# Optimization experiments

Measured on AMD Instinct MI355X. Metric: run time of the kernel, lower is better.

## Reference

```python
import jax, jax.numpy as jnp
import numpy as np

# dims: F=N_fault, V=N_train (noise samples), E=batch, M=n_in+2, N=n_out
F, V, E, N_IN, N_OUT = 2, 4, 2048, 512, 512
M = N_IN + 2
GMIN, GMAX, EPS_TRAIN, PGMIN = 0.01, 10.0, 0.1, 1e-4
ETA2_ACT1 = 0.20  # ACT1.eta_fault[0,2], used in theta init
# pTanh activation params per ACT: a = e0 + e1*tanh((z-e2)*e3)
ETAS = np.array([[0.05, 0.90, 0.20, 8.0],
                 [0.10, 0.80, 0.30, 5.0],
                 [0.00, 1.00, 0.25, 10.0],
                 [0.15, 0.70, 0.15, 6.0]], dtype=np.float32)


def setup_inputs() -> dict:
    key = jax.random.key(0)
    k1, k2, k3, k4, k5 = jax.random.split(key, 5)
    a_previous = jax.random.uniform(k1, (F, V, E, N_IN), jnp.float32)
    # theta init per __init__: rand/100 + gmin; last row += gmax; row -2 from eta_2 formula
    theta = jax.random.uniform(k2, (M, N_OUT), jnp.float32) / 100.0 + GMIN
    theta = theta.at[-1, :].add(GMAX)
    theta = theta.at[-2, :].set(ETA2_ACT1 / (1.0 - ETA2_ACT1) * (jnp.sum(theta[:-2, :], 0) + theta[-1, :]))
    cofficients_act = jax.random.uniform(k3, (4, N_OUT), jnp.float32)
    noise_u = jax.random.uniform(k4, (F, V, M, N_OUT), jnp.float32)   # theta_noisy uniform draw
    gumbel_u = jax.random.uniform(k5, (4, N_OUT), jnp.float32)        # gumbel uniform draw
    return {"a_previous": a_previous, "theta_": theta,
            "cofficients_act": cofficients_act, "noise_u": noise_u, "gumbel_u": gumbel_u}


def _forward(a_previous, theta_, cofficients_act, noise_u, gumbel_u):
    sg = jax.lax.stop_gradient
    # --- theta property: clamp to [-gmax,gmax], zero |.|<gmin, straight-through ---
    th_c = jnp.clip(theta_, -GMAX, GMAX)
    th_t = jnp.where(jnp.abs(th_c) < GMIN, 0.0, th_c)
    theta = sg(th_t) + theta_ - sg(theta_)
    # --- theta_noisy: multiplicative uniform noise in [1-eps, 1+eps]; FaultMask == 1 ---
    theta_noisy = theta[None, None] * ((noise_u * 2.0 - 1.0) * EPS_TRAIN + 1.0)  # [F,V,M,N]
    absn = jnp.abs(theta_noisy)
    W = absn / (jnp.sum(absn, axis=2, keepdims=True) + 1e-10)
    pos = (theta_noisy >= 0).astype(theta_noisy.dtype)
    neg = 1.0 - pos
    # --- MAC: extend input with [ones, zeros], inverter path, split-sign matmul ---
    ones = jnp.ones(a_previous.shape[:3] + (1,), a_previous.dtype)
    zeros = jnp.zeros_like(ones)
    x_ext = jnp.concatenate([a_previous, ones, zeros], axis=3)  # [F,V,E,M]
    x_neg = (-x_ext).at[..., -1].set(0.0)                       # ideal INV(a) = -a, last col zeroed
    z = (jnp.einsum('fvem,fvmn->fven', x_ext, W * pos)
         + jnp.einsum('fvem,fvmn->fven', x_neg, W * neg))       # [F,V,E,N]
    # --- MAC_power: vectorized form of the quad loop ---
    # Power = sum_{f,v,m,n} g[m,n] * sum_e (x_ext*pos + x_neg*neg - y)^2 / (E*V*F)
    # pos*neg = 0, pos^2 = pos  =>  expand the square into einsum reductions.
    g_init = jnp.abs(th_c)
    g_tilde = g_init * (PGMIN / jnp.min(g_init, axis=0, keepdims=True))
    pos_d, neg_d = sg(pos), sg(neg)  # detached in torch source
    sx2 = jnp.einsum('fvem,fvem->fvm', x_ext, x_ext)
    sn2 = jnp.einsum('fvem,fvem->fvm', x_neg, x_neg)
    sy2 = jnp.einsum('fven,fven->fvn', z, z)
    C = jnp.einsum('fvem,fven->fvmn', x_ext, z)
    D = jnp.einsum('fvem,fven->fvmn', x_neg, z)
    p1 = (jnp.einsum('fvm,fvmn,mn->', sx2, pos_d, g_tilde)
          + jnp.einsum('fvm,fvmn,mn->', sn2, neg_d, g_tilde))
    p2 = -2.0 * (jnp.einsum('fvmn,fvmn,mn->', C, pos_d, g_tilde)
                 + jnp.einsum('fvmn,fvmn,mn->', D, neg_d, g_tilde))
    p3 = jnp.einsum('fvn,n->', sy2, jnp.sum(g_tilde, axis=0))
    mac_power = (p1 + p2 + p3) / (E * V * F)
    # --- CoFF_ACT: clamped logits + gumbel, softmax, hard argmax straight-through ---
    c = cofficients_act + sg(jnp.clip(cofficients_act, -1.0, 1.0) - cofficients_act)
    gn = -jnp.log(-jnp.log(gumbel_u + 1e-20) + 1e-20)
    alpha = jax.nn.softmax((c + gn) / 1.0, axis=0)              # temperature = 1.0
    hard = jax.nn.one_hot(jnp.argmax(alpha, axis=0), 4, axis=0, dtype=alpha.dtype)
    alpha_st = sg(hard) + alpha - sg(alpha)                      # [4, N]
    # --- mix the four pTanh activations ---
    a_new = jnp.zeros_like(z)
    for i in range(4):
        e0, e1, e2, e3 = ETAS[i]
        a_new = a_new + alpha_st[i] * (e0 + e1 * jnp.tanh((z - e2) * e3))
    return a_new, mac_power


def reference(a_previous, theta_, cofficients_act, noise_u, gumbel_u):
    return _forward(a_previous, theta_, cofficients_act, noise_u, gumbel_u)
```

## Files before the change

### kernel.cpp

```cpp
#include <hip/hip_runtime.h>

typedef unsigned short u16;
typedef __attribute__((ext_vector_type(8))) short short8;
typedef __attribute__((ext_vector_type(4))) float f32x4;

#define NF 2
#define NV 4
#define FV 8
#define NE 2048
#define NIN 512
#define NOUT 512
#define NM 514

#define WS_P1      0u
#define WS_P2      2048u
#define WS_P3      3072u
#define WS_SCALE   4096u
#define WS_G       6144u
#define WS_GN      8320u
#define WS_ETA     10368u
#define WS_BIASZ   18560u
#define WS_BIAST   34944u
#define WS_DENP    51328u
#define WS_PMIN    133248u
#define WS_PSUM    264320u
#define WS_ABF     395392u
#define WS_BZT     17172608u
#define WS_BTT     21366912u

__constant__ float c_etas[4][4] = {
    {0.05f, 0.90f, 0.20f, 8.0f},
    {0.10f, 0.80f, 0.30f, 5.0f},
    {0.00f, 1.00f, 0.25f, 10.0f},
    {0.15f, 0.70f, 0.15f, 6.0f}};

__device__ __forceinline__ u16 f2bf(float x) {
    unsigned u = __float_as_uint(x);
    unsigned r = (u + 0x7fffu + ((u >> 16) & 1u)) >> 16;
    return (u16)r;
}

__device__ __forceinline__ void gll16(const void* g, void* l) {
    __builtin_amdgcn_global_load_lds((__attribute__((address_space(1))) void*)g,
                                     (__attribute__((address_space(3))) void*)l,
                                     16, 0, 0);
}

__global__ void kA_part(const float* __restrict__ theta_, float* __restrict__ pmin,
                        float* __restrict__ psum) {
    int t = threadIdx.x;
    int n2 = t * 2;
    int r0 = blockIdx.x * 9;
    float mn0 = 3.4e38f, mn1 = 3.4e38f, s0 = 0.f, s1 = 0.f;
    int rend = r0 + 9;
    if (rend > NM) rend = NM;
    for (int r = r0; r < rend; r++) {
        float2 v = *(const float2*)(theta_ + r * NOUT + n2);
        float a0 = fabsf(fminf(fmaxf(v.x, -10.f), 10.f));
        float a1 = fabsf(fminf(fmaxf(v.y, -10.f), 10.f));
        mn0 = fminf(mn0, a0); mn1 = fminf(mn1, a1);
        s0 += a0; s1 += a1;
    }
    *(float2*)(pmin + blockIdx.x * NOUT + n2) = make_float2(mn0, mn1);
    *(float2*)(psum + blockIdx.x * NOUT + n2) = make_float2(s0, s1);
}

__global__ void kB_fold(const float* __restrict__ pmin, const float* __restrict__ psum,
                        const float* __restrict__ coeff, const float* __restrict__ gumb,
                        float* __restrict__ scale, float* __restrict__ Gn,
                        float4* __restrict__ eta4) {
    int n = threadIdx.x;
    float mn = 3.4e38f, s = 0.f;
    for (int i = 0; i < 64; i++) {
        mn = fminf(mn, pmin[i * NOUT + n]);
        s += psum[i * NOUT + n];
    }
    float sc = 1e-4f / mn;
    scale[n] = sc;
    Gn[n] = sc * s;
    float best = -1e30f;
    int bi = 0;
    for (int i = 0; i < 4; i++) {
        float c = fminf(fmaxf(coeff[i * NOUT + n], -1.f), 1.f);
        float u = gumb[i * NOUT + n];
        float g = -logf(-logf(u + 1e-20f) + 1e-20f);
        float v = c + g;
        if (v > best) { best = v; bi = i; }
    }
    eta4[n] = make_float4(c_etas[bi][0], c_etas[bi][1], c_etas[bi][2], c_etas[bi][3]);
}

__global__ void kC_grow(const float* __restrict__ theta_, const float* __restrict__ scale,
                        float* __restrict__ G) {
    int m = blockIdx.x;
    int t = threadIdx.x;
    const float4* rowp = (const float4*)(theta_ + m * NOUT);
    const float4* scp = (const float4*)scale;
    float acc = 0.f;
#pragma unroll
    for (int i = 0; i < 2; i++) {
        float4 v = rowp[t * 2 + i];
        float4 s = scp[t * 2 + i];
        acc += fabsf(fminf(fmaxf(v.x, -10.f), 10.f)) * s.x
             + fabsf(fminf(fmaxf(v.y, -10.f), 10.f)) * s.y
             + fabsf(fminf(fmaxf(v.z, -10.f), 10.f)) * s.z
             + fabsf(fminf(fmaxf(v.w, -10.f), 10.f)) * s.w;
    }
    for (int off = 32; off > 0; off >>= 1) acc += __shfl_down(acc, off);
    if (t == 0) G[m] = acc;
}

__global__ void k_denomp(const float* __restrict__ theta_, const float* __restrict__ noise,
                         float* __restrict__ denomp) {
    int fv = blockIdx.z, mc = blockIdx.y, nc = blockIdx.x;
    int t = threadIdx.x;
    int nl = t & 63, mg = t >> 6;
    int n = nc * 64 + nl;
    int mbase = mc * 128 + mg * 32;
    float acc = 0.f;
    for (int i = 0; i < 32; i++) {
        int m = mbase + i;
        if (m < NM) {
            float fac = noise[(fv * NM + m) * NOUT + n] * 0.2f + 0.9f;
            float thc = fminf(fmaxf(theta_[m * NOUT + n], -10.f), 10.f);
            float tht = (fabsf(thc) < 0.01f) ? 0.f : thc;
            acc += fabsf(tht * fac);
        }
    }
    __shared__ float red[4][64];
    red[mg][nl] = acc;
    __syncthreads();
    if (t < 64)
        denomp[(mc * FV + fv) * NOUT + nc * 64 + t] =
            red[0][t] + red[1][t] + red[2][t] + red[3][t];
}

__global__ void k_wmat3(const float* __restrict__ theta_, const float* __restrict__ scale,
                        const float* __restrict__ noise, const float* __restrict__ denomp,
                        u16* __restrict__ BzT, u16* __restrict__ BtT,
                        float* __restrict__ bias_z, float* __restrict__ bias_t) {
    int fv = blockIdx.z, mt = blockIdx.y, nt = blockIdx.x;
    int t = threadIdx.x;
    int nl = t & 63, rg = t >> 6;
    __shared__ u16 Wl[64][66];
    __shared__ u16 Sl[64][66];
    int n = nt * 64 + nl;
    float dsum = 1e-10f;
#pragma unroll
    for (int mc = 0; mc < 5; mc++) dsum += denomp[(mc * FV + fv) * NOUT + n];
    float rdv = 1.f / dsum;
    float sc = scale[n];
    for (int r = 0; r < 16; r++) {
        int ml = rg * 16 + r;
        int m = mt * 64 + ml;
        if (m < 513) {
            float fac = noise[(fv * NM + m) * NOUT + n] * 0.2f + 0.9f;
            float thc = fminf(fmaxf(theta_[m * NOUT + n], -10.f), 10.f);
            float gi = fabsf(thc);
            float tht = (gi < 0.01f) ? 0.f : thc;
            float th = tht * fac;
            float sg = (th >= 0.f) ? 1.f : -1.f;
            float gt = gi * sc;
            if (m == 512) {
                bias_z[fv * NOUT + n] = th * rdv;
                bias_t[fv * NOUT + n] = sg * gt;
            } else {
                Wl[ml][nl] = f2bf(th * rdv);
                Sl[ml][nl] = f2bf(sg * gt);
            }
        }
    }
    __syncthreads();
    if (mt < 8) {
        for (int r = 0; r < 16; r++) {
            int nl2 = rg * 16 + r;
            int ml2 = t & 63;
            int gidx = (fv * NOUT + nt * 64 + nl2) * NIN + mt * 64 + ml2;
            BzT[gidx] = Wl[ml2][nl2];
            BtT[gidx] = Sl[ml2][nl2];
        }
    }
}

__global__ void k_prepA(const float* __restrict__ a_prev, const float* __restrict__ G,
                        u16* __restrict__ Abf, float* __restrict__ p1slot) {
    int t = threadIdx.x;
    float acc = 0.f;
#pragma unroll
    for (int i = 0; i < 4; i++) {
        int idx = (i * 2048 + blockIdx.x) * 256 + t;
        float4 v = ((const float4*)a_prev)[idx];
        int k = (idx & 127) << 2;
        float4 g4 = *((const float4*)(G + k));
        acc += v.x * v.x * g4.x + v.y * v.y * g4.y + v.z * v.z * g4.z + v.w * v.w * g4.w;
        ushort4 o;
        o.x = f2bf(v.x); o.y = f2bf(v.y); o.z = f2bf(v.z); o.w = f2bf(v.w);
        ((ushort4*)Abf)[idx] = o;
    }
    for (int off = 32; off > 0; off >>= 1) acc += __shfl_down(acc, off);
    __shared__ float red[4];
    int lane = t & 63, wv = t >> 6;
    if (lane == 0) red[wv] = acc;
    __syncthreads();
    if (t == 0)
        atomicAdd(&p1slot[(blockIdx.x & 63) * 8], red[0] + red[1] + red[2] + red[3]);
}

__global__ __launch_bounds__(256, 2) void k_gemm(
    const u16* __restrict__ Abf, const u16* __restrict__ BzT, const u16* __restrict__ BtT,
    const float* __restrict__ bias_z, const float* __restrict__ bias_t,
    const float* __restrict__ Gn, const float4* __restrict__ eta4,
    float* __restrict__ out, float* __restrict__ p2slot, float* __restrict__ p3slot) {
    __shared__ alignas(16) u16 As[128 * 64];
    __shared__ alignas(16) u16 Bzs[128 * 64];
    __shared__ alignas(16) u16 Bts[128 * 64];
    const int tid = threadIdx.x;
    const int lane = tid & 63;
    const int wv = tid >> 6;
    const int wr = wv >> 1, wc = wv & 1;
    const int fv = blockIdx.z;
    const int e0 = blockIdx.y * 128;
    const int n0 = blockIdx.x * 128;

    const u16* Ag = Abf + (fv * NE + e0) * NIN;
    const u16* Bzg = BzT + (fv * NOUT + n0) * NIN;
    const u16* Btg = BtT + (fv * NOUT + n0) * NIN;

    f32x4 accz[4][4], acct[4][4];
#pragma unroll
    for (int i = 0; i < 4; i++)
#pragma unroll
        for (int j = 0; j < 4; j++) {
            f32x4 zz = {0.f, 0.f, 0.f, 0.f};
            accz[i][j] = zz;
            acct[i][j] = zz;
        }

    const int srow = tid >> 3;
    const int swz = (((tid & 7) ^ (srow & 7))) * 8;

    for (int k0 = 0; k0 < 512; k0 += 64) {
#pragma unroll
        for (int i = 0; i < 4; i++) {
            int so = (i * 32 + srow) * 512 + k0 + swz;
            int dof = i * 2048 + tid * 8;
            gll16(Ag + so, (u16*)As + dof);
            gll16(Bzg + so, (u16*)Bzs + dof);
            gll16(Btg + so, (u16*)Bts + dof);
        }
        __builtin_amdgcn_s_waitcnt(0);
        __syncthreads();
        const int rA = wr * 64 + (lane & 15);
        const int rB = wc * 64 + (lane & 15);
#pragma unroll
        for (int s = 0; s < 2; s++) {
            const int ca = ((s * 4 + (lane >> 4)) ^ (lane & 7)) * 8;
            short8 af[4], bzf[4], btf[4];
#pragma unroll
            for (int i = 0; i < 4; i++) af[i] = *(const short8*)(As + (rA + i * 16) * 64 + ca);
#pragma unroll
            for (int j = 0; j < 4; j++) {
                bzf[j] = *(const short8*)(Bzs + (rB + j * 16) * 64 + ca);
                btf[j] = *(const short8*)(Bts + (rB + j * 16) * 64 + ca);
            }
#pragma unroll
            for (int i = 0; i < 4; i++)
#pragma unroll
                for (int j = 0; j < 4; j++) {
                    accz[i][j] = __builtin_amdgcn_mfma_f32_16x16x32_bf16(af[i], bzf[j], accz[i][j], 0, 0, 0);
                    acct[i][j] = __builtin_amdgcn_mfma_f32_16x16x32_bf16(af[i], btf[j], acct[i][j], 0, 0, 0);
                }
        }
        __syncthreads();
    }

    float p2 = 0.f, p3 = 0.f;
    const int col = lane & 15;
    const int rowq = (lane >> 4) * 4;
#pragma unroll
    for (int j = 0; j < 4; j++) {
        int n = n0 + wc * 64 + j * 16 + col;
        float bz = bias_z[fv * NOUT + n];
        float bt = bias_t[fv * NOUT + n];
        float gnv = Gn[n];
        float4 e4 = eta4[n];
#pragma unroll
        for (int i = 0; i < 4; i++) {
            int ebase = e0 + wr * 64 + i * 16 + rowq;
#pragma unroll
            for (int r = 0; r < 4; r++) {
                float z = accz[i][j][r] + bz;
                float t = acct[i][j][r] + bt;
                p2 += z * t;
                p3 += z * z * gnv;
                float x = (z - e4.z) * e4.w;
                float ex = __expf(2.f * x);
                float th = 1.f - 2.f / (ex + 1.f);
                out[(fv * NE + ebase + r) * NOUT + n] = e4.x + e4.y * th;
            }
        }
    }
    for (int off = 32; off > 0; off >>= 1) {
        p2 += __shfl_down(p2, off);
        p3 += __shfl_down(p3, off);
    }
    __shared__ float r2[4], r3[4];
    if (lane == 0) { r2[wv] = p2; r3[wv] = p3; }
    __syncthreads();
    if (tid == 0) {
        int slot = ((blockIdx.x + blockIdx.y * 4 + blockIdx.z * 64) & 31) * 8;
        atomicAdd(&p2slot[slot], r2[0] + r2[1] + r2[2] + r2[3]);
        atomicAdd(&p3slot[slot], r3[0] + r3[1] + r3[2] + r3[3]);
    }
}

__global__ void k_final(const float* __restrict__ p1s, const float* __restrict__ p2s,
                        const float* __restrict__ p3s, const float* __restrict__ G,
                        float* __restrict__ out) {
    int t = threadIdx.x;
    float s1 = p1s[t * 8];
    float s2 = (t < 32) ? p2s[t * 8] : 0.f;
    float s3 = (t < 32) ? p3s[t * 8] : 0.f;
    for (int off = 32; off > 0; off >>= 1) {
        s1 += __shfl_down(s1, off);
        s2 += __shfl_down(s2, off);
        s3 += __shfl_down(s3, off);
    }
    if (t == 0) {
        float mp = (s1 + 16384.f * G[512] - 2.f * s2 + s3) * (1.f / 16384.f);
        out[8388608] = mp;
    }
}

extern "C" void kernel_launch(void* const* d_in, const int* in_sizes, int n_in,
                              void* d_out, int out_size, void* d_ws, size_t ws_size,
                              hipStream_t stream) {
    const float* a_prev = (const float*)d_in[0];
    const float* theta_ = (const float*)d_in[1];
    const float* coeff = (const float*)d_in[2];
    const float* noise = (const float*)d_in[3];
    const float* gumb = (const float*)d_in[4];
    float* out = (float*)d_out;
    char* w = (char*)d_ws;
    float* p1s = (float*)(w + WS_P1);
    float* p2s = (float*)(w + WS_P2);
    float* p3s = (float*)(w + WS_P3);
    float* scale = (float*)(w + WS_SCALE);
    float* G = (float*)(w + WS_G);
    float* Gn = (float*)(w + WS_GN);
    float4* eta4 = (float4*)(w + WS_ETA);
    float* bias_z = (float*)(w + WS_BIASZ);
    float* bias_t = (float*)(w + WS_BIAST);
    float* denomp = (float*)(w + WS_DENP);
    float* pmin = (float*)(w + WS_PMIN);
    float* psum = (float*)(w + WS_PSUM);
    u16* Abf = (u16*)(w + WS_ABF);
    u16* BzT = (u16*)(w + WS_BZT);
    u16* BtT = (u16*)(w + WS_BTT);

    hipMemsetAsync(w + WS_P1, 0, 4096, stream);

    kA_part<<<64, 256, 0, stream>>>(theta_, pmin, psum);
    kB_fold<<<1, 512, 0, stream>>>(pmin, psum, coeff, gumb, scale, Gn, eta4);
    kC_grow<<<514, 64, 0, stream>>>(theta_, scale, G);
    k_denomp<<<dim3(8, 5, FV), 256, 0, stream>>>(theta_, noise, denomp);
    k_wmat3<<<dim3(8, 9, FV), 256, 0, stream>>>(theta_, scale, noise, denomp,
                                                BzT, BtT, bias_z, bias_t);
    k_prepA<<<2048, 256, 0, stream>>>(a_prev, G, Abf, p1s);
    k_gemm<<<dim3(4, 16, FV), 256, 0, stream>>>(Abf, BzT, BtT, bias_z, bias_t, Gn, eta4,
                                                out, p2s, p3s);
    k_final<<<1, 64, 0, stream>>>(p1s, p2s, p3s, G, out);
}
```

Baseline: 153.1 us.

## Defer column normalization to GEMM epilogue and vectorize weight prep kernels

```diff
diff --git a/kernel.cpp b/kernel.cpp
--- a/kernel.cpp
+++ b/kernel.cpp
@@ -22,11 +22,11 @@
 #define WS_BIASZ   18560u
 #define WS_BIAST   34944u
 #define WS_DENP    51328u
-#define WS_PMIN    133248u
-#define WS_PSUM    264320u
-#define WS_ABF     395392u
-#define WS_BZT     17172608u
-#define WS_BTT     21366912u
+#define WS_PMIN    182400u
+#define WS_PSUM    313472u
+#define WS_ABF     444544u
+#define WS_BZT     17221760u
+#define WS_BTT     21416064u
 
 __constant__ float c_etas[4][4] = {
     {0.05f, 0.90f, 0.20f, 8.0f},
@@ -112,73 +112,88 @@
 
 __global__ void k_denomp(const float* __restrict__ theta_, const float* __restrict__ noise,
                          float* __restrict__ denomp) {
-    int fv = blockIdx.z, mc = blockIdx.y, nc = blockIdx.x;
-    int t = threadIdx.x;
-    int nl = t & 63, mg = t >> 6;
-    int n = nc * 64 + nl;
-    int mbase = mc * 128 + mg * 32;
-    float acc = 0.f;
-    for (int i = 0; i < 32; i++) {
-        int m = mbase + i;
-        if (m < NM) {
-            float fac = noise[(fv * NM + m) * NOUT + n] * 0.2f + 0.9f;
-            float thc = fminf(fmaxf(theta_[m * NOUT + n], -10.f), 10.f);
-            float tht = (fabsf(thc) < 0.01f) ? 0.f : thc;
-            acc += fabsf(tht * fac);
-        }
-    }
-    __shared__ float red[4][64];
-    red[mg][nl] = acc;
+    const int fv = blockIdx.z, mc = blockIdx.y, nc = blockIdx.x;
+    const int t = threadIdx.x;
+    const int nq = t & 15, mr = t >> 4;
+    const int nb = nc * 64 + nq * 4;
+    float4 acc = {0.f, 0.f, 0.f, 0.f};
+#pragma unroll
+    for (int i = 0; i < 4; i++) {
+        int m = mc * 64 + mr + i * 16;
+        float4 th4 = *(const float4*)(theta_ + m * NOUT + nb);
+        float4 no4 = *(const float4*)(noise + (fv * NM + m) * NOUT + nb);
+#define DACC(c) { float fac = no4.c * 0.2f + 0.9f; \
+                  float thc = fminf(fmaxf(th4.c, -10.f), 10.f); \
+                  float tht = (fabsf(thc) < 0.01f) ? 0.f : thc; \
+                  acc.c += fabsf(tht * fac); }
+        DACC(x) DACC(y) DACC(z) DACC(w)
+#undef DACC
+    }
+    __shared__ float4 red[16][17];
+    red[mr][nq] = acc;
     __syncthreads();
-    if (t < 64)
-        denomp[(mc * FV + fv) * NOUT + nc * 64 + t] =
-            red[0][t] + red[1][t] + red[2][t] + red[3][t];
+    if (t < 16) {
+        float4 s = red[0][t];
+#pragma unroll
+        for (int r = 1; r < 16; r++) {
+            float4 v = red[r][t];
+            s.x += v.x; s.y += v.y; s.z += v.z; s.w += v.w;
+        }
+        *(float4*)(denomp + (mc * 8 + fv) * NOUT + nc * 64 + t * 4) = s;
+    }
 }
 
 __global__ void k_wmat3(const float* __restrict__ theta_, const float* __restrict__ scale,
-                        const float* __restrict__ noise, const float* __restrict__ denomp,
+                        const float* __restrict__ noise,
                         u16* __restrict__ BzT, u16* __restrict__ BtT,
                         float* __restrict__ bias_z, float* __restrict__ bias_t) {
-    int fv = blockIdx.z, mt = blockIdx.y, nt = blockIdx.x;
-    int t = threadIdx.x;
-    int nl = t & 63, rg = t >> 6;
-    __shared__ u16 Wl[64][66];
-    __shared__ u16 Sl[64][66];
-    int n = nt * 64 + nl;
-    float dsum = 1e-10f;
-#pragma unroll
-    for (int mc = 0; mc < 5; mc++) dsum += denomp[(mc * FV + fv) * NOUT + n];
-    float rdv = 1.f / dsum;
-    float sc = scale[n];
-    for (int r = 0; r < 16; r++) {
-        int ml = rg * 16 + r;
+    const int nt = blockIdx.x, mt = blockIdx.y, fv = blockIdx.z;
+    const int t = threadIdx.x;
+    const int nq = t & 15, mr = t >> 4;
+    const int nb = nt * 64 + nq * 4;
+    __shared__ u16 Wl[64][72];
+    __shared__ u16 Sl[64][72];
+    float4 sc4 = *(const float4*)(scale + nb);
+#pragma unroll
+    for (int i = 0; i < 4; i++) {
+        int ml = mr + i * 16;
         int m = mt * 64 + ml;
-        if (m < 513) {
-            float fac = noise[(fv * NM + m) * NOUT + n] * 0.2f + 0.9f;
-            float thc = fminf(fmaxf(theta_[m * NOUT + n], -10.f), 10.f);
-            float gi = fabsf(thc);
-            float tht = (gi < 0.01f) ? 0.f : thc;
-            float th = tht * fac;
-            float sg = (th >= 0.f) ? 1.f : -1.f;
-            float gt = gi * sc;
-            if (m == 512) {
-                bias_z[fv * NOUT + n] = th * rdv;
-                bias_t[fv * NOUT + n] = sg * gt;
-            } else {
-                Wl[ml][nl] = f2bf(th * rdv);
-                Sl[ml][nl] = f2bf(sg * gt);
-            }
-        }
+        float4 th4 = *(const float4*)(theta_ + m * NOUT + nb);
+        float4 no4 = *(const float4*)(noise + (fv * NM + m) * NOUT + nb);
+        ushort4 wv, sv;
+#define WCOMP(c, fld) { float fac = no4.c * 0.2f + 0.9f; \
+                        float thc = fminf(fmaxf(th4.c, -10.f), 10.f); \
+                        float gi = fabsf(thc); \
+                        float tht = (gi < 0.01f) ? 0.f : thc; \
+                        float th = tht * fac; \
+                        wv.fld = f2bf(th); \
+                        sv.fld = f2bf(((th >= 0.f) ? 1.f : -1.f) * gi * sc4.c); }
+        WCOMP(x, x) WCOMP(y, y) WCOMP(z, z) WCOMP(w, w)
+#undef WCOMP
+        *(ushort4*)(&Wl[ml][nq * 4]) = wv;
+        *(ushort4*)(&Sl[ml][nq * 4]) = sv;
     }
     __syncthreads();
-    if (mt < 8) {
-        for (int r = 0; r < 16; r++) {
-            int nl2 = rg * 16 + r;
-            int ml2 = t & 63;
-            int gidx = (fv * NOUT + nt * 64 + nl2) * NIN + mt * 64 + ml2;
-            BzT[gidx] = Wl[ml2][nl2];
-            BtT[gidx] = Sl[ml2][nl2];
-        }
+    const int mb = (t & 15) * 4;
+#pragma unroll
+    for (int r = 0; r < 4; r++) {
+        int nl = (t >> 4) + r * 16;
+        ushort4 wv, sv;
+        wv.x = Wl[mb][nl]; wv.y = Wl[mb + 1][nl]; wv.z = Wl[mb + 2][nl]; wv.w = Wl[mb + 3][nl];
+        sv.x = Sl[mb][nl]; sv.y = Sl[mb + 1][nl]; sv.z = Sl[mb + 2][nl]; sv.w = Sl[mb + 3][nl];
+        int gidx = (fv * NOUT + nt * 64 + nl) * NIN + mt * 64 + mb;
+        *(ushort4*)(BzT + gidx) = wv;
+        *(ushort4*)(BtT + gidx) = sv;
+    }
+    if (mt == 0 && t < 64) {
+        int n = nt * 64 + t;
+        float fac = noise[(fv * NM + 512) * NOUT + n] * 0.2f + 0.9f;
+        float thc = fminf(fmaxf(theta_[512 * NOUT + n], -10.f), 10.f);
+        float gi = fabsf(thc);
+        float tht = (gi < 0.01f) ? 0.f : thc;
+        float th = tht * fac;
+        bias_z[fv * NOUT + n] = th;
+        bias_t[fv * NOUT + n] = ((th >= 0.f) ? 1.f : -1.f) * gi * scale[n];
     }
 }
 
@@ -210,6 +225,8 @@
     const u16* __restrict__ Abf, const u16* __restrict__ BzT, const u16* __restrict__ BtT,
     const float* __restrict__ bias_z, const float* __restrict__ bias_t,
     const float* __restrict__ Gn, const float4* __restrict__ eta4,
+    const float* __restrict__ theta_, const float* __restrict__ noise,
+    const float* __restrict__ denomp,
     float* __restrict__ out, float* __restrict__ p2slot, float* __restrict__ p3slot) {
     __shared__ alignas(16) u16 As[128 * 64];
     __shared__ alignas(16) u16 Bzs[128 * 64];
@@ -280,6 +297,17 @@
 #pragma unroll
     for (int j = 0; j < 4; j++) {
         int n = n0 + wc * 64 + j * 16 + col;
+        float dsum = 1e-10f;
+#pragma unroll
+        for (int mc = 0; mc < 8; mc++) dsum += denomp[(mc * 8 + fv) * NOUT + n];
+#pragma unroll
+        for (int mx = 512; mx < 514; mx++) {
+            float fac = noise[(fv * NM + mx) * NOUT + n] * 0.2f + 0.9f;
+            float thc = fminf(fmaxf(theta_[mx * NOUT + n], -10.f), 10.f);
+            float tht = (fabsf(thc) < 0.01f) ? 0.f : thc;
+            dsum += fabsf(tht * fac);
+        }
+        float rdv = 1.f / dsum;
         float bz = bias_z[fv * NOUT + n];
         float bt = bias_t[fv * NOUT + n];
         float gnv = Gn[n];
@@ -289,7 +317,7 @@
             int ebase = e0 + wr * 64 + i * 16 + rowq;
 #pragma unroll
             for (int r = 0; r < 4; r++) {
-                float z = accz[i][j][r] + bz;
+                float z = (accz[i][j][r] + bz) * rdv;
                 float t = acct[i][j][r] + bt;
                 p2 += z * t;
                 p3 += z * z * gnv;
@@ -363,11 +391,11 @@
     kA_part<<<64, 256, 0, stream>>>(theta_, pmin, psum);
     kB_fold<<<1, 512, 0, stream>>>(pmin, psum, coeff, gumb, scale, Gn, eta4);
     kC_grow<<<514, 64, 0, stream>>>(theta_, scale, G);
-    k_denomp<<<dim3(8, 5, FV), 256, 0, stream>>>(theta_, noise, denomp);
-    k_wmat3<<<dim3(8, 9, FV), 256, 0, stream>>>(theta_, scale, noise, denomp,
+    k_denomp<<<dim3(8, 8, FV), 256, 0, stream>>>(theta_, noise, denomp);
+    k_wmat3<<<dim3(8, 8, FV), 256, 0, stream>>>(theta_, scale, noise,
                                                 BzT, BtT, bias_z, bias_t);
     k_prepA<<<2048, 256, 0, stream>>>(a_prev, G, Abf, p1s);
     k_gemm<<<dim3(4, 16, FV), 256, 0, stream>>>(Abf, BzT, BtT, bias_z, bias_t, Gn, eta4,
-                                                out, p2s, p3s);
+                                                theta_, noise, denomp, out, p2s, p3s);
     k_final<<<1, 64, 0, stream>>>(p1s, p2s, p3s, G, out);
 }
```

New measurement: 146.3 us. 1.05x faster.
